# Kernel tuning notes

Hardware: AMD Instinct MI355X
Metric: run time of the kernel (lower is better)

## Reference

```python
import jax, jax.numpy as jnp
import numpy as np

H = 4  # num_heads (hard-coded in module)
RATION = 5


def setup_inputs() -> dict:
    key = jax.random.key(0)
    ks = jax.random.split(key, 14)
    B, T, S, F = 256, 5, 64, 256
    u = 0.05  # keras 'uniform' initializer scale
    d = {}
    d["x"] = jax.random.normal(ks[0], (B, T, S, F), jnp.float32)
    d["atten_bias"] = jax.random.uniform(ks[1], (B, T, S, S), jnp.float32) * 0.1
    d["W_q"] = jax.random.uniform(ks[2], (F, F), jnp.float32, -u, u)
    d["W_v"] = jax.random.uniform(ks[3], (F, F), jnp.float32, -u, u)
    d["W_o"] = jax.random.uniform(ks[4], (F, F), jnp.float32, -u, u)
    d["u_t"] = jax.random.uniform(ks[5], (T,), jnp.float32, -u, u)
    d["dis"] = jax.random.uniform(ks[6], (T, S, S), jnp.float32, -u, u)
    # keep sigma away from 0 to avoid blowing up the Gaussian prior
    d["sigma"] = jax.random.uniform(ks[7], (T, S, 1), jnp.float32, 0.5, 1.0)
    # SE block: fc1 Dense(T*RATION, relu, he_normal), fc2 Dense(T, sigmoid)
    d["fc1_w"] = jax.random.normal(ks[8], (T, T * RATION), jnp.float32) * np.sqrt(2.0 / T).astype(np.float32)
    d["fc1_b"] = jnp.zeros((T * RATION,), jnp.float32)
    d["fc2_w"] = jax.random.normal(ks[9], (T * RATION, T), jnp.float32) * np.sqrt(2.0 / (T * RATION)).astype(np.float32)
    d["fc2_b"] = jnp.zeros((T,), jnp.float32)
    d["bili_w"] = jax.random.uniform(ks[10], (1,), jnp.float32, -u, u)
    return d


def _se_block(o, fc1_w, fc1_b, fc2_w, fc2_b, bili_w):
    # o: [B,T,S,F] -> transpose to [B,S,F,T]; "channel" axis is T
    xt = jnp.transpose(o, (0, 2, 3, 1))
    avg = jnp.mean(xt, axis=(1, 2))  # [B,T]
    mx = jnp.max(xt, axis=(1, 2))    # [B,T]
    se1 = jax.nn.sigmoid(jax.nn.relu(avg @ fc1_w + fc1_b) @ fc2_w + fc2_b)
    se2 = jax.nn.sigmoid(jax.nn.relu(mx @ fc1_w + fc1_b) @ fc2_w + fc2_b)
    w = bili_w  # shape (1,)
    se = (1.0 - w) * se1 + w * se2   # [B,T]
    out = xt * se[:, None, None, :]
    return jnp.transpose(out, (0, 3, 1, 2))  # back to [B,T,S,F]


def reference(x, atten_bias, W_q, W_v, W_o, u_t, dis, sigma, fc1_w, fc1_b, fc2_w, fc2_b, bili_w):
    B, T, S, F = x.shape
    Fh = F // H
    # q, v: project then reshape (row-major split, exactly as TF reshape)
    q = (x @ W_q).reshape(-1, T, S, Fh)          # [H*B, T, S, Fh]
    v = (x @ W_v).reshape(-1, T, S, Fh)          # [H*B, T, S, Fh]
    # k: contract time with u_t, then [B,F,S] -> [H*B, Fh, S]
    k = jnp.einsum('t,btsf->bsf', u_t, x)        # [B, S, F]
    k = jnp.transpose(k, (0, 2, 1)).reshape(-1, Fh, S)  # [H*B, Fh, S]
    score = jnp.einsum('btsf,bfc->btsc', q, k) / jnp.sqrt(jnp.asarray(Fh, x.dtype))
    score = jax.nn.sigmoid(score)                # [H*B, T, S, S]
    score = score - jnp.tile(atten_bias, (H, 1, 1, 1))
    # learned spatial Gaussian prior, broadcast over batch
    prior = (1.0 / (jnp.sqrt(2.0 * jnp.pi) * sigma)) * jnp.exp(-dis ** 2 / (2.0 * sigma ** 2))
    score = score * prior
    # Dropout(0.3) is identity at inference
    score = jnp.sum(score, axis=-2)              # [H*B, T, S]
    atten = v * score[..., None]                 # [H*B, T, S, Fh]
    o = atten.reshape(-1, T, S, F) @ W_o         # [B, T, S, F]
    o = _se_block(o, fc1_w, fc1_b, fc2_w, fc2_b, bili_w)
    return o + x
```

## Files before the change

kernel.cpp:

```cpp
#include <hip/hip_runtime.h>


typedef unsigned short ushort_t;
typedef __attribute__((ext_vector_type(8))) short bf16x8;
typedef __attribute__((ext_vector_type(4))) float f32x4;

__device__ inline ushort_t f2bf(float f) {
  unsigned u = __float_as_uint(f);
  return (ushort_t)((u + 0x7FFFu + ((u >> 16) & 1u)) >> 16);
}
__device__ inline float bflo(unsigned u) { return __uint_as_float(u << 16); }
__device__ inline float bfhi(unsigned u) { return __uint_as_float(u & 0xFFFF0000u); }

__global__ __launch_bounds__(256) void prep_kernel(
    const float* __restrict__ x, const float* __restrict__ u,
    const float* __restrict__ Wq, const float* __restrict__ Wv,
    const float* __restrict__ Wo, const float* __restrict__ dis,
    const float* __restrict__ sigma, const float* __restrict__ bias,
    ushort_t* __restrict__ Wt, float* __restrict__ prior,
    float* __restrict__ bps, ushort_t* __restrict__ kout,
    ushort_t* __restrict__ xb) {
  __shared__ float red[4][64];
  const int blk = blockIdx.x, tid = threadIdx.x;
  if (blk < 768) {
    int id = blk * 256 + tid;
    int mat = id >> 16, rem = id & 65535;
    int n = rem >> 8, k = rem & 255;
    const float* W = mat == 0 ? Wq : (mat == 1 ? Wv : Wo);
    Wt[id] = f2bf(W[k * 256 + n]);
  } else if (blk < 848) {
    int i = (blk - 768) * 256 + tid;
    int ts = i >> 6;
    float sg = sigma[ts];
    float d = dis[i];
    prior[i] = 0.3989422804014327f / sg * __expf(-d * d / (2.f * sg * sg));
  } else if (blk < 2128) {
    int b2 = blk - 848;
    int t = b2 % 5;
    const float* bp = bias + (size_t)b2 * 4096;
    int c = tid & 63, sg_ = tid >> 6;
    float sum = 0.f;
    for (int s = sg_ * 16; s < sg_ * 16 + 16; ++s) {
      float sgm = sigma[t * 64 + s];
      float d = dis[t * 4096 + s * 64 + c];
      float pr = 0.3989422804014327f / sgm * __expf(-d * d / (2.f * sgm * sgm));
      sum += bp[s * 64 + c] * pr;
    }
    red[sg_][c] = sum;
    __syncthreads();
    if (tid < 64)
      bps[(size_t)b2 * 64 + tid] = red[0][tid] + red[1][tid] + red[2][tid] + red[3][tid];
  } else {
    int i = (blk - 2128) * 256 + tid;
    size_t j = (size_t)i * 4;
    int b = (int)(j >> 14);
    int off = (int)(j & 16383);
    const float* xp = x + (size_t)b * 81920 + off;
    ushort_t* xq = xb + (size_t)b * 81920 + off;
    float u0 = u[0], u1 = u[1], u2 = u[2], u3 = u[3], u4 = u[4];
    float4 a0 = *(const float4*)(xp);
    float4 a1 = *(const float4*)(xp + 16384);
    float4 a2 = *(const float4*)(xp + 32768);
    float4 a3 = *(const float4*)(xp + 49152);
    float4 a4 = *(const float4*)(xp + 65536);
    ushort4 h0 = {f2bf(a0.x), f2bf(a0.y), f2bf(a0.z), f2bf(a0.w)};
    ushort4 h1 = {f2bf(a1.x), f2bf(a1.y), f2bf(a1.z), f2bf(a1.w)};
    ushort4 h2 = {f2bf(a2.x), f2bf(a2.y), f2bf(a2.z), f2bf(a2.w)};
    ushort4 h3 = {f2bf(a3.x), f2bf(a3.y), f2bf(a3.z), f2bf(a3.w)};
    ushort4 h4 = {f2bf(a4.x), f2bf(a4.y), f2bf(a4.z), f2bf(a4.w)};
    *(ushort4*)(xq) = h0;
    *(ushort4*)(xq + 16384) = h1;
    *(ushort4*)(xq + 32768) = h2;
    *(ushort4*)(xq + 49152) = h3;
    *(ushort4*)(xq + 65536) = h4;
    float4 r;
    r.x = u0 * a0.x + u1 * a1.x + u2 * a2.x + u3 * a3.x + u4 * a4.x;
    r.y = u0 * a0.y + u1 * a1.y + u2 * a2.y + u3 * a3.y + u4 * a4.y;
    r.z = u0 * a0.z + u1 * a1.z + u2 * a2.z + u3 * a3.z + u4 * a4.z;
    r.w = u0 * a0.w + u1 * a1.w + u2 * a2.w + u3 * a3.w + u4 * a4.w;
    ushort4 h = {f2bf(r.x), f2bf(r.y), f2bf(r.z), f2bf(r.w)};
    *(ushort4*)(kout + j) = h;
  }
}

template<int SCALE, int SEEPI>
__global__ __launch_bounds__(512, 4) void gemm_mfma(
    const ushort_t* __restrict__ A, const ushort_t* __restrict__ Wt,
    ushort_t* C, const float* __restrict__ ssum,
    float* __restrict__ ravg, float* __restrict__ rmax) {
  __shared__ __align__(16) ushort_t As_[128 * 64];
  __shared__ __align__(16) ushort_t Bs_[256 * 64];
  __shared__ float redS[8], redM[8];
  const int tid = threadIdx.x;
  const int lane = tid & 63;
  const int w = tid >> 6, wr = w >> 2, wc = w & 3;
  const int row0 = blockIdx.x * 128;
  const int cl = lane & 15, ql = lane >> 4, l7 = lane & 7;

  f32x4 acc[4][4];
#pragma unroll
  for (int i = 0; i < 4; ++i)
#pragma unroll
    for (int j = 0; j < 4; ++j) acc[i][j] = (f32x4){0.f, 0.f, 0.f, 0.f};

  for (int t = 0; t < 4; ++t) {
    const int k0 = t * 64;
    if (t) __syncthreads();
#pragma unroll
    for (int l = 0; l < 2; ++l) {
      int i = l * 512 + tid;
      int r = i >> 3, c = i & 7;
      uint4 v = *(const uint4*)(A + (size_t)(row0 + r) * 256 + k0 + c * 8);
      *(uint4*)&As_[r * 64 + ((c ^ (r & 7)) * 8)] = v;
    }
#pragma unroll
    for (int l = 0; l < 4; ++l) {
      int i = l * 512 + tid;
      int n = i >> 3, c = i & 7;
      uint4 v = *(const uint4*)(Wt + (size_t)n * 256 + k0 + c * 8);
      *(uint4*)&Bs_[n * 64 + ((c ^ (n & 7)) * 8)] = v;
    }
    __syncthreads();
#pragma unroll
    for (int kk = 0; kk < 2; ++kk) {
      const int offk = (((kk << 2) | ql) ^ l7) * 8;
      bf16x8 bfr[4], afr[4];
#pragma unroll
      for (int ni = 0; ni < 4; ++ni)
        bfr[ni] = *(const bf16x8*)&Bs_[(wc * 64 + ni * 16 + cl) * 64 + offk];
#pragma unroll
      for (int mi = 0; mi < 4; ++mi)
        afr[mi] = *(const bf16x8*)&As_[(wr * 64 + mi * 16 + cl) * 64 + offk];
#pragma unroll
      for (int mi = 0; mi < 4; ++mi)
#pragma unroll
        for (int ni = 0; ni < 4; ++ni)
          acc[mi][ni] = __builtin_amdgcn_mfma_f32_16x16x32_bf16(afr[mi], bfr[ni], acc[mi][ni], 0, 0, 0);
    }
  }
  float lsum = 0.f, lmax = -3.4e38f;
#pragma unroll
  for (int mi = 0; mi < 4; ++mi) {
    float sc[4];
    if (SCALE) {
#pragma unroll
      for (int r = 0; r < 4; ++r)
        sc[r] = ssum[(size_t)(row0 + wr * 64 + mi * 16 + ql * 4 + r) * 4 + wc];
    }
#pragma unroll
    for (int ni = 0; ni < 4; ++ni) {
      int col = wc * 64 + ni * 16 + cl;
      f32x4 v = acc[mi][ni];
#pragma unroll
      for (int r = 0; r < 4; ++r) {
        int row = row0 + wr * 64 + mi * 16 + ql * 4 + r;
        float f = v[r];
        if (SCALE) f *= sc[r];
        C[(size_t)row * 256 + col] = f2bf(f);
        if (SEEPI) { lsum += f; lmax = fmaxf(lmax, f); }
      }
    }
  }
  if (SEEPI) {
#pragma unroll
    for (int off = 32; off; off >>= 1) {
      lsum += __shfl_xor(lsum, off);
      lmax = fmaxf(lmax, __shfl_xor(lmax, off));
    }
    if (lane == 0) { redS[w] = lsum; redM[w] = lmax; }
    __syncthreads();
    if (tid < 2) {
      float s = redS[tid * 4] + redS[tid * 4 + 1] + redS[tid * 4 + 2] + redS[tid * 4 + 3];
      float m = fmaxf(fmaxf(redM[tid * 4], redM[tid * 4 + 1]),
                      fmaxf(redM[tid * 4 + 2], redM[tid * 4 + 3]));
      ravg[blockIdx.x * 2 + tid] = s * (1.f / 16384.f);
      rmax[blockIdx.x * 2 + tid] = m;
    }
  }
}

__global__ __launch_bounds__(256) void score_mfma(const ushort_t* __restrict__ q,
                                                  const ushort_t* __restrict__ kbuf,
                                                  const float* __restrict__ prior,
                                                  const float* __restrict__ bps,
                                                  float* __restrict__ ssum) {
  const int n = blockIdx.x;
  const int tid = threadIdx.x;
  const int lane = tid & 63;
  const int w = tid >> 6;
  const int cl = lane & 15, ql = lane >> 4;
  const int nb = n & 255;
  const int c = w * 16 + cl;
  const ushort_t* kb = kbuf + (size_t)(n >> 2) * 16384 + (n & 3) * 64;
  bf16x8 kfr0 = *(const bf16x8*)(kb + c * 256 + ql * 8);
  bf16x8 kfr1 = *(const bf16x8*)(kb + c * 256 + ql * 8 + 32);
  for (int t = 0; t < 5; ++t) {
    const ushort_t* qt = q + (size_t)n * 20480 + t * 4096;
    f32x4 acc[4];
#pragma unroll
    for (int si = 0; si < 4; ++si) {
      bf16x8 a0 = *(const bf16x8*)(qt + (si * 16 + cl) * 64 + ql * 8);
      bf16x8 a1 = *(const bf16x8*)(qt + (si * 16 + cl) * 64 + ql * 8 + 32);
      f32x4 z = (f32x4){0.f, 0.f, 0.f, 0.f};
      z = __builtin_amdgcn_mfma_f32_16x16x32_bf16(a0, kfr0, z, 0, 0, 0);
      z = __builtin_amdgcn_mfma_f32_16x16x32_bf16(a1, kfr1, z, 0, 0, 0);
      acc[si] = z;
    }
    const float* pp = prior + t * 4096;
    float colsum = 0.f;
#pragma unroll
    for (int si = 0; si < 4; ++si) {
#pragma unroll
      for (int r = 0; r < 4; ++r) {
        int s = si * 16 + ql * 4 + r;
        float sg = 1.f / (1.f + __expf(-acc[si][r] * 0.125f));
        colsum += sg * pp[s * 64 + c];
      }
    }
    colsum += __shfl_xor(colsum, 16);
    colsum += __shfl_xor(colsum, 32);
    if (ql == 0)
      ssum[(size_t)n * 320 + t * 64 + c] = colsum - bps[((size_t)nb * 5 + t) * 64 + c];
  }
}

__global__ __launch_bounds__(256) void final_kernel(
    const ushort_t* __restrict__ xb, const ushort_t* __restrict__ ob,
    const float* __restrict__ ravg, const float* __restrict__ rmax,
    const float* __restrict__ fc1w, const float* __restrict__ fc1b,
    const float* __restrict__ fc2w, const float* __restrict__ fc2b,
    const float* __restrict__ bili, float* __restrict__ out) {
  __shared__ float sse;
  int i = blockIdx.x * 256 + threadIdx.x;
  size_t j = (size_t)i * 4;
  int bt = (int)(j >> 14);
  uint2 uo = *(const uint2*)(ob + j);
  uint2 ux = *(const uint2*)(xb + j);
  if (threadIdx.x == 0) {
    int b = bt / 5, t = bt % 5;
    float avg[5], mx[5];
    for (int tt = 0; tt < 5; ++tt) { avg[tt] = ravg[b * 5 + tt]; mx[tt] = rmax[b * 5 + tt]; }
    float w = bili[0];
    float s12[2];
    for (int p = 0; p < 2; ++p) {
      const float* in = p == 0 ? avg : mx;
      float a = fc2b[t];
      for (int jj = 0; jj < 25; ++jj) {
        float hh = fc1b[jj];
        for (int tt = 0; tt < 5; ++tt) hh += in[tt] * fc1w[tt * 25 + jj];
        a += fmaxf(hh, 0.f) * fc2w[jj * 5 + t];
      }
      s12[p] = 1.f / (1.f + __expf(-a));
    }
    sse = (1.f - w) * s12[0] + w * s12[1];
  }
  __syncthreads();
  float s = sse;
  float4 r = {bflo(uo.x) * s + bflo(ux.x), bfhi(uo.x) * s + bfhi(ux.x),
              bflo(uo.y) * s + bflo(ux.y), bfhi(uo.y) * s + bfhi(ux.y)};
  *(float4*)(out + j) = r;
}

extern "C" void kernel_launch(void* const* d_in, const int* in_sizes, int n_in,
                              void* d_out, int out_size, void* d_ws, size_t ws_size,
                              hipStream_t stream) {
  const float* x     = (const float*)d_in[0];
  const float* bias  = (const float*)d_in[1];
  const float* Wq    = (const float*)d_in[2];
  const float* Wv    = (const float*)d_in[3];
  const float* Wo    = (const float*)d_in[4];
  const float* u_t   = (const float*)d_in[5];
  const float* dis   = (const float*)d_in[6];
  const float* sigma = (const float*)d_in[7];
  const float* fc1w  = (const float*)d_in[8];
  const float* fc1b  = (const float*)d_in[9];
  const float* fc2w  = (const float*)d_in[10];
  const float* fc2b  = (const float*)d_in[11];
  const float* bili  = (const float*)d_in[12];
  float* out = (float*)d_out;

  char* wsb = (char*)d_ws;
  ushort_t* xbuf = (ushort_t*)wsb;             wsb += 41943040;
  ushort_t* qvb  = (ushort_t*)wsb;             wsb += 41943040;
  ushort_t* kb   = (ushort_t*)wsb;             wsb += 8388608;
  ushort_t* Wt   = (ushort_t*)wsb;             wsb += 393216;
  float*    ssum = (float*)wsb;                wsb += 1310720;
  float*    prior= (float*)wsb;                wsb += 81920;
  float*    bps  = (float*)wsb;                wsb += 327680;
  float*    ravg = (float*)wsb;                wsb += 5120;
  float*    rmax = (float*)wsb;                wsb += 5120;

  prep_kernel<<<6224, 256, 0, stream>>>(x, u_t, Wq, Wv, Wo, dis, sigma, bias,
                                        Wt, prior, bps, kb, xbuf);
  gemm_mfma<0, 0><<<640, 512, 0, stream>>>(xbuf, Wt, qvb, nullptr, nullptr, nullptr);
  score_mfma<<<1024, 256, 0, stream>>>(qvb, kb, prior, bps, ssum);
  gemm_mfma<1, 0><<<640, 512, 0, stream>>>(xbuf, Wt + 65536, qvb, ssum, nullptr, nullptr);
  gemm_mfma<0, 1><<<640, 512, 0, stream>>>(qvb, Wt + 131072, qvb, nullptr, ravg, rmax);
  final_kernel<<<20480, 256, 0, stream>>>(xbuf, qvb, ravg, rmax,
                                          fc1w, fc1b, fc2w, fc2b, bili, out);
}
```

Measured before the change: 166.8 us.

## Fuse Q projection GEMM into score kernel and widen x conversion vectors

Replaces the separate Q-projection GEMM and score kernel with one kernel. Each block computes its 320x64 slice of x@W_q with MFMA, stages the result as bf16 in LDS, and immediately applies the sigmoid-score and prior column sum. This avoids writing Q to global memory and reading it back. The prep kernel's x-to-bf16 and k-contraction path now handles 8 elements per thread with 16-byte stores, cutting its block count. The trade-off is that each fused block reloads W_q tiles, so W_q traffic becomes redundant across the 1024 blocks, and the fused kernel has higher register and LDS pressure.

```diff
diff --git a/kernel.cpp b/kernel.cpp
--- a/kernel.cpp
+++ b/kernel.cpp
@@ -11,6 +11,14 @@
 }
 __device__ inline float bflo(unsigned u) { return __uint_as_float(u << 16); }
 __device__ inline float bfhi(unsigned u) { return __uint_as_float(u & 0xFFFF0000u); }
+__device__ inline uint4 pack8(float4 a, float4 b) {
+  uint4 r;
+  r.x = (unsigned)f2bf(a.x) | ((unsigned)f2bf(a.y) << 16);
+  r.y = (unsigned)f2bf(a.z) | ((unsigned)f2bf(a.w) << 16);
+  r.z = (unsigned)f2bf(b.x) | ((unsigned)f2bf(b.y) << 16);
+  r.w = (unsigned)f2bf(b.z) | ((unsigned)f2bf(b.w) << 16);
+  return r;
+}
 
 __global__ __launch_bounds__(256) void prep_kernel(
     const float* __restrict__ x, const float* __restrict__ u,
@@ -52,34 +60,135 @@
       bps[(size_t)b2 * 64 + tid] = red[0][tid] + red[1][tid] + red[2][tid] + red[3][tid];
   } else {
     int i = (blk - 2128) * 256 + tid;
-    size_t j = (size_t)i * 4;
+    size_t j = (size_t)i * 8;
     int b = (int)(j >> 14);
     int off = (int)(j & 16383);
     const float* xp = x + (size_t)b * 81920 + off;
     ushort_t* xq = xb + (size_t)b * 81920 + off;
     float u0 = u[0], u1 = u[1], u2 = u[2], u3 = u[3], u4 = u[4];
-    float4 a0 = *(const float4*)(xp);
-    float4 a1 = *(const float4*)(xp + 16384);
-    float4 a2 = *(const float4*)(xp + 32768);
-    float4 a3 = *(const float4*)(xp + 49152);
-    float4 a4 = *(const float4*)(xp + 65536);
-    ushort4 h0 = {f2bf(a0.x), f2bf(a0.y), f2bf(a0.z), f2bf(a0.w)};
-    ushort4 h1 = {f2bf(a1.x), f2bf(a1.y), f2bf(a1.z), f2bf(a1.w)};
-    ushort4 h2 = {f2bf(a2.x), f2bf(a2.y), f2bf(a2.z), f2bf(a2.w)};
-    ushort4 h3 = {f2bf(a3.x), f2bf(a3.y), f2bf(a3.z), f2bf(a3.w)};
-    ushort4 h4 = {f2bf(a4.x), f2bf(a4.y), f2bf(a4.z), f2bf(a4.w)};
-    *(ushort4*)(xq) = h0;
-    *(ushort4*)(xq + 16384) = h1;
-    *(ushort4*)(xq + 32768) = h2;
-    *(ushort4*)(xq + 49152) = h3;
-    *(ushort4*)(xq + 65536) = h4;
-    float4 r;
-    r.x = u0 * a0.x + u1 * a1.x + u2 * a2.x + u3 * a3.x + u4 * a4.x;
-    r.y = u0 * a0.y + u1 * a1.y + u2 * a2.y + u3 * a3.y + u4 * a4.y;
-    r.z = u0 * a0.z + u1 * a1.z + u2 * a2.z + u3 * a3.z + u4 * a4.z;
-    r.w = u0 * a0.w + u1 * a1.w + u2 * a2.w + u3 * a3.w + u4 * a4.w;
-    ushort4 h = {f2bf(r.x), f2bf(r.y), f2bf(r.z), f2bf(r.w)};
-    *(ushort4*)(kout + j) = h;
+    float4 lo[5], hi[5];
+#pragma unroll
+    for (int t = 0; t < 5; ++t) {
+      lo[t] = *(const float4*)(xp + t * 16384);
+      hi[t] = *(const float4*)(xp + t * 16384 + 4);
+    }
+#pragma unroll
+    for (int t = 0; t < 5; ++t)
+      *(uint4*)(xq + t * 16384) = pack8(lo[t], hi[t]);
+    float4 rl, rh;
+    rl.x = u0*lo[0].x + u1*lo[1].x + u2*lo[2].x + u3*lo[3].x + u4*lo[4].x;
+    rl.y = u0*lo[0].y + u1*lo[1].y + u2*lo[2].y + u3*lo[3].y + u4*lo[4].y;
+    rl.z = u0*lo[0].z + u1*lo[1].z + u2*lo[2].z + u3*lo[3].z + u4*lo[4].z;
+    rl.w = u0*lo[0].w + u1*lo[1].w + u2*lo[2].w + u3*lo[3].w + u4*lo[4].w;
+    rh.x = u0*hi[0].x + u1*hi[1].x + u2*hi[2].x + u3*hi[3].x + u4*hi[4].x;
+    rh.y = u0*hi[0].y + u1*hi[1].y + u2*hi[2].y + u3*hi[3].y + u4*hi[4].y;
+    rh.z = u0*hi[0].z + u1*hi[1].z + u2*hi[2].z + u3*hi[3].z + u4*hi[4].z;
+    rh.w = u0*hi[0].w + u1*hi[1].w + u2*hi[2].w + u3*hi[3].w + u4*hi[4].w;
+    *(uint4*)(kout + j) = pack8(rl, rh);
+  }
+}
+
+__global__ __launch_bounds__(256) void qscore(const ushort_t* __restrict__ xb,
+                                              const ushort_t* __restrict__ Wtq,
+                                              const ushort_t* __restrict__ kbuf,
+                                              const float* __restrict__ prior,
+                                              const float* __restrict__ bps,
+                                              float* __restrict__ ssum) {
+  __shared__ __align__(16) char smem[46080];
+  ushort_t* As_ = (ushort_t*)smem;
+  ushort_t* Bs_ = (ushort_t*)(smem + 10240);
+  ushort_t* qlds = (ushort_t*)smem;
+  const int n = blockIdx.x;
+  const int tid = threadIdx.x;
+  const int lane = tid & 63, w = tid >> 6;
+  const int cl = lane & 15, ql = lane >> 4, l7 = lane & 7;
+  const ushort_t* A = xb + (size_t)n * 20480;
+
+  const int c = w * 16 + cl;
+  const int nb = n & 255;
+  const ushort_t* kbp = kbuf + (size_t)(n >> 2) * 16384 + (n & 3) * 64;
+  bf16x8 kfr0 = *(const bf16x8*)(kbp + c * 256 + ql * 8);
+  bf16x8 kfr1 = *(const bf16x8*)(kbp + c * 256 + ql * 8 + 32);
+
+  f32x4 acc[5][4];
+#pragma unroll
+  for (int mi = 0; mi < 5; ++mi)
+#pragma unroll
+    for (int ni = 0; ni < 4; ++ni) acc[mi][ni] = (f32x4){0.f, 0.f, 0.f, 0.f};
+
+  for (int t4 = 0; t4 < 4; ++t4) {
+    const int k0 = t4 * 64;
+    if (t4) __syncthreads();
+#pragma unroll
+    for (int l = 0; l < 3; ++l) {
+      int i = l * 256 + tid;
+      if (i < 640) {
+        int r = i >> 3, cc = i & 7;
+        uint4 v = *(const uint4*)(A + (size_t)r * 256 + k0 + cc * 8);
+        *(uint4*)&As_[r * 64 + ((cc ^ (r & 7)) * 8)] = v;
+      }
+    }
+#pragma unroll
+    for (int l = 0; l < 8; ++l) {
+      int i = l * 256 + tid;
+      int nn = i >> 3, cc = i & 7;
+      uint4 v = *(const uint4*)(Wtq + (size_t)nn * 256 + k0 + cc * 8);
+      *(uint4*)&Bs_[nn * 64 + ((cc ^ (nn & 7)) * 8)] = v;
+    }
+    __syncthreads();
+#pragma unroll
+    for (int kk = 0; kk < 2; ++kk) {
+      const int offk = (((kk << 2) | ql) ^ l7) * 8;
+      bf16x8 bfr[4];
+#pragma unroll
+      for (int ni = 0; ni < 4; ++ni)
+        bfr[ni] = *(const bf16x8*)&Bs_[(w * 64 + ni * 16 + cl) * 64 + offk];
+#pragma unroll
+      for (int mi = 0; mi < 5; ++mi) {
+        bf16x8 afr = *(const bf16x8*)&As_[(mi * 16 + cl) * 64 + offk];
+#pragma unroll
+        for (int ni = 0; ni < 4; ++ni)
+          acc[mi][ni] = __builtin_amdgcn_mfma_f32_16x16x32_bf16(afr, bfr[ni], acc[mi][ni], 0, 0, 0);
+      }
+    }
+  }
+  __syncthreads();
+#pragma unroll
+  for (int mi = 0; mi < 5; ++mi)
+#pragma unroll
+    for (int ni = 0; ni < 4; ++ni)
+#pragma unroll
+      for (int rr = 0; rr < 4; ++rr)
+        qlds[(mi * 64 + 16 * ql + 4 * rr + w) * 72 + ni * 16 + cl] = f2bf(acc[mi][ni][rr]);
+  __syncthreads();
+
+#pragma unroll
+  for (int t = 0; t < 5; ++t) {
+    f32x4 sacc[4];
+#pragma unroll
+    for (int si = 0; si < 4; ++si) {
+      bf16x8 a0 = *(const bf16x8*)&qlds[(t * 64 + si * 16 + cl) * 72 + ql * 8];
+      bf16x8 a1 = *(const bf16x8*)&qlds[(t * 64 + si * 16 + cl) * 72 + ql * 8 + 32];
+      f32x4 z = (f32x4){0.f, 0.f, 0.f, 0.f};
+      z = __builtin_amdgcn_mfma_f32_16x16x32_bf16(a0, kfr0, z, 0, 0, 0);
+      z = __builtin_amdgcn_mfma_f32_16x16x32_bf16(a1, kfr1, z, 0, 0, 0);
+      sacc[si] = z;
+    }
+    const float* pp = prior + t * 4096;
+    float colsum = 0.f;
+#pragma unroll
+    for (int si = 0; si < 4; ++si) {
+#pragma unroll
+      for (int r = 0; r < 4; ++r) {
+        int s = si * 16 + ql * 4 + r;
+        float sg = 1.f / (1.f + __expf(-sacc[si][r] * 0.125f));
+        colsum += sg * pp[s * 64 + c];
+      }
+    }
+    colsum += __shfl_xor(colsum, 16);
+    colsum += __shfl_xor(colsum, 32);
+    if (ql == 0)
+      ssum[(size_t)n * 320 + t * 64 + c] = colsum - bps[((size_t)nb * 5 + t) * 64 + c];
   }
 }
 
@@ -176,51 +285,6 @@
       ravg[blockIdx.x * 2 + tid] = s * (1.f / 16384.f);
       rmax[blockIdx.x * 2 + tid] = m;
     }
-  }
-}
-
-__global__ __launch_bounds__(256) void score_mfma(const ushort_t* __restrict__ q,
-                                                  const ushort_t* __restrict__ kbuf,
-                                                  const float* __restrict__ prior,
-                                                  const float* __restrict__ bps,
-                                                  float* __restrict__ ssum) {
-  const int n = blockIdx.x;
-  const int tid = threadIdx.x;
-  const int lane = tid & 63;
-  const int w = tid >> 6;
-  const int cl = lane & 15, ql = lane >> 4;
-  const int nb = n & 255;
-  const int c = w * 16 + cl;
-  const ushort_t* kb = kbuf + (size_t)(n >> 2) * 16384 + (n & 3) * 64;
-  bf16x8 kfr0 = *(const bf16x8*)(kb + c * 256 + ql * 8);
-  bf16x8 kfr1 = *(const bf16x8*)(kb + c * 256 + ql * 8 + 32);
-  for (int t = 0; t < 5; ++t) {
-    const ushort_t* qt = q + (size_t)n * 20480 + t * 4096;
-    f32x4 acc[4];
-#pragma unroll
-    for (int si = 0; si < 4; ++si) {
-      bf16x8 a0 = *(const bf16x8*)(qt + (si * 16 + cl) * 64 + ql * 8);
-      bf16x8 a1 = *(const bf16x8*)(qt + (si * 16 + cl) * 64 + ql * 8 + 32);
-      f32x4 z = (f32x4){0.f, 0.f, 0.f, 0.f};
-      z = __builtin_amdgcn_mfma_f32_16x16x32_bf16(a0, kfr0, z, 0, 0, 0);
-      z = __builtin_amdgcn_mfma_f32_16x16x32_bf16(a1, kfr1, z, 0, 0, 0);
-      acc[si] = z;
-    }
-    const float* pp = prior + t * 4096;
-    float colsum = 0.f;
-#pragma unroll
-    for (int si = 0; si < 4; ++si) {
-#pragma unroll
-      for (int r = 0; r < 4; ++r) {
-        int s = si * 16 + ql * 4 + r;
-        float sg = 1.f / (1.f + __expf(-acc[si][r] * 0.125f));
-        colsum += sg * pp[s * 64 + c];
-      }
-    }
-    colsum += __shfl_xor(colsum, 16);
-    colsum += __shfl_xor(colsum, 32);
-    if (ql == 0)
-      ssum[(size_t)n * 320 + t * 64 + c] = colsum - bps[((size_t)nb * 5 + t) * 64 + c];
   }
 }
 
@@ -290,10 +354,9 @@
   float*    ravg = (float*)wsb;                wsb += 5120;
   float*    rmax = (float*)wsb;                wsb += 5120;
 
-  prep_kernel<<<6224, 256, 0, stream>>>(x, u_t, Wq, Wv, Wo, dis, sigma, bias,
+  prep_kernel<<<4176, 256, 0, stream>>>(x, u_t, Wq, Wv, Wo, dis, sigma, bias,
                                         Wt, prior, bps, kb, xbuf);
-  gemm_mfma<0, 0><<<640, 512, 0, stream>>>(xbuf, Wt, qvb, nullptr, nullptr, nullptr);
-  score_mfma<<<1024, 256, 0, stream>>>(qvb, kb, prior, bps, ssum);
+  qscore<<<1024, 256, 0, stream>>>(xbuf, Wt, kb, prior, bps, ssum);
   gemm_mfma<1, 0><<<640, 512, 0, stream>>>(xbuf, Wt + 65536, qvb, ssum, nullptr, nullptr);
   gemm_mfma<0, 1><<<640, 512, 0, stream>>>(qvb, Wt + 131072, qvb, nullptr, ravg, rmax);
   final_kernel<<<20480, 256, 0, stream>>>(xbuf, qvb, ravg, rmax,
```

Measured after the change: 156.2 us. 6.3% less time.
